# Performance work log

Measured on AMD Instinct MI355X. Metric: run time of the kernel, lower is better.

Reference implementation:

```python
import jax, jax.numpy as jnp
import numpy as np

B, L, D, H = 2, 2048, 1024, 16
Dh = D // H            # 64
DIL = 2                # dilation
WIN = 256              # window_size
HID = 4 * D            # ffn hidden (mlp_ratio=4.0)
EPS = 1e-5             # LayerNorm eps (torch default)


def _layernorm(x, w, b):
    m = jnp.mean(x, axis=-1, keepdims=True)
    v = jnp.mean(jnp.square(x - m), axis=-1, keepdims=True)
    return (x - m) * jax.lax.rsqrt(v + EPS) * w + b


def _dilated_mask(L):
    i = jnp.arange(L)[:, None]
    j = jnp.arange(L)[None, :]
    d = i - j
    return (jnp.remainder(d, DIL) == 0) & (jnp.abs(d) <= WIN) & (j <= i)  # [L,L] bool, True=allowed


def setup_inputs() -> dict:
    key = jax.random.key(0)
    ks = jax.random.split(key, 16)
    s = 0.02
    return {
        "x": jax.random.normal(ks[0], (B, L, D), jnp.float32),
        "norm1_w": jnp.ones((D,), jnp.float32),
        "norm1_b": jnp.zeros((D,), jnp.float32),
        "qkv_w": jax.random.normal(ks[1], (D, 3 * D), jnp.float32) * s,
        "qkv_b": jnp.zeros((3 * D,), jnp.float32),
        "out_w": jax.random.normal(ks[2], (D, D), jnp.float32) * s,
        "out_b": jnp.zeros((D,), jnp.float32),
        "norm2_w": jnp.ones((D,), jnp.float32),
        "norm2_b": jnp.zeros((D,), jnp.float32),
        "ffn_w1": jax.random.normal(ks[3], (D, HID), jnp.float32) * s,
        "ffn_b1": jnp.zeros((HID,), jnp.float32),
        "ffn_w2": jax.random.normal(ks[4], (HID, D), jnp.float32) * s,
        "ffn_b2": jnp.zeros((D,), jnp.float32),
    }


def reference(x, norm1_w, norm1_b, qkv_w, qkv_b, out_w, out_b,
              norm2_w, norm2_b, ffn_w1, ffn_b1, ffn_w2, ffn_b2):
    # pre-norm dilated attention block
    xn = _layernorm(x, norm1_w, norm1_b)
    qkv = xn @ qkv_w + qkv_b                         # [B,L,3D]
    q, k, v = jnp.split(qkv, 3, axis=-1)
    to_h = lambda t: t.reshape(B, L, H, Dh).transpose(0, 2, 1, 3)  # [B,H,L,Dh]
    qh, kh, vh = to_h(q), to_h(k), to_h(v)

    scale = 1.0 / jnp.sqrt(jnp.float32(Dh))
    scores = jnp.einsum('bhqd,bhkd->bhqk', qh, kh) * scale  # [B,H,L,L]
    allowed = _dilated_mask(L)                               # [L,L]
    scores = jnp.where(allowed[None, None], scores, jnp.float32(-1e30))
    p = jax.nn.softmax(scores, axis=-1)
    o = jnp.einsum('bhqk,bhkd->bhqd', p, vh)                 # [B,H,L,Dh]
    o = o.transpose(0, 2, 1, 3).reshape(B, L, D)
    attn_out = o @ out_w + out_b

    y = x + attn_out                                          # residual (dropout=0)
    h = _layernorm(y, norm2_w, norm2_b)
    h = jax.nn.gelu(h @ ffn_w1 + ffn_b1, approximate=False) @ ffn_w2 + ffn_b2
    return y + h
```

## Files before the change

kernel.cpp:

```cpp
#include <hip/hip_runtime.h>
#include <math.h>

#define BB 2
#define LL 2048
#define DD 1024
#define HH 16
#define DH 64
#define HID 4096
#define MROWS (BB*LL)

typedef __attribute__((ext_vector_type(8))) short bf16x8;
typedef __attribute__((ext_vector_type(4))) float f32x4;

__device__ __forceinline__ unsigned short f2bf(float f) {
    unsigned u = __builtin_bit_cast(unsigned, f);
    unsigned r = u + 0x7fffu + ((u >> 16) & 1u);
    return (unsigned short)(r >> 16);
}

__device__ __forceinline__ void ldsload16(const void* g, void* l) {
    __builtin_amdgcn_global_load_lds(
        (const __attribute__((address_space(1))) unsigned int*)g,
        (__attribute__((address_space(3))) unsigned int*)l,
        16, 0, 0);
}

__global__ __launch_bounds__(256) void convT_kernel(const float* __restrict__ in,
                                                    unsigned short* __restrict__ out,
                                                    int K, int N) {
    __shared__ float tile[64][65];
    int kt = blockIdx.y << 6, nt = blockIdx.x << 6;
    int t = threadIdx.x;
    int tr = t >> 4;
    int tc = (t & 15) << 2;
    #pragma unroll
    for (int i = 0; i < 4; ++i) {
        float4 v = *reinterpret_cast<const float4*>(&in[(size_t)(kt + i*16 + tr) * N + nt + tc]);
        tile[i*16 + tr][tc+0] = v.x;
        tile[i*16 + tr][tc+1] = v.y;
        tile[i*16 + tr][tc+2] = v.z;
        tile[i*16 + tr][tc+3] = v.w;
    }
    __syncthreads();
    #pragma unroll
    for (int i = 0; i < 4; ++i) {
        int n = i*16 + tr;
        ushort4 o4;
        o4.x = f2bf(tile[tc+0][n]);
        o4.y = f2bf(tile[tc+1][n]);
        o4.z = f2bf(tile[tc+2][n]);
        o4.w = f2bf(tile[tc+3][n]);
        *reinterpret_cast<ushort4*>(&out[(size_t)(nt + n) * K + kt + tc]) = o4;
    }
}

__global__ __launch_bounds__(256) void ln_kernel(const float* __restrict__ in,
                                                 const float* __restrict__ w,
                                                 const float* __restrict__ b,
                                                 unsigned short* __restrict__ out) {
    int row = blockIdx.x;
    const float* x = in + (size_t)row * DD;
    unsigned short* o = out + (size_t)row * DD;
    int t = threadIdx.x;
    float4 v = reinterpret_cast<const float4*>(x)[t];
    float s  = v.x + v.y + v.z + v.w;
    float ss = v.x*v.x + v.y*v.y + v.z*v.z + v.w*v.w;
    #pragma unroll
    for (int off = 32; off > 0; off >>= 1) {
        s  += __shfl_down(s,  off, 64);
        ss += __shfl_down(ss, off, 64);
    }
    __shared__ float red[8];
    int wid = t >> 6, lane = t & 63;
    if (lane == 0) { red[wid] = s; red[4 + wid] = ss; }
    __syncthreads();
    if (t == 0) {
        float S  = red[0] + red[1] + red[2] + red[3];
        float SS = red[4] + red[5] + red[6] + red[7];
        float mean = S / DD;
        float var  = SS / DD - mean * mean;
        red[0] = mean;
        red[1] = rsqrtf(var + 1e-5f);
    }
    __syncthreads();
    float mean = red[0], rstd = red[1];
    float4 wv = reinterpret_cast<const float4*>(w)[t];
    float4 bv = reinterpret_cast<const float4*>(b)[t];
    ushort4 ov;
    ov.x = f2bf((v.x - mean) * rstd * wv.x + bv.x);
    ov.y = f2bf((v.y - mean) * rstd * wv.y + bv.y);
    ov.z = f2bf((v.z - mean) * rstd * wv.z + bv.z);
    ov.w = f2bf((v.w - mean) * rstd * wv.w + bv.w);
    reinterpret_cast<ushort4*>(o)[t] = ov;
}

template<int EPI>
__global__ __launch_bounds__(256) void mgemm(
    const unsigned short* __restrict__ A,
    const unsigned short* __restrict__ WT,
    const float* __restrict__ bias,
    const float* res, void* Cv,
    int M, int N, int K, int nbx)
{
    __shared__ __align__(16) unsigned char smem[32768];
    int bid = blockIdx.x;
    int nwg = gridDim.x;
    int cpx = nwg >> 3;
    int swz = (bid & 7) * cpx + (bid >> 3);
    int bn = (swz % nbx) * 128;
    int bm = (swz / nbx) * 128;
    int t = threadIdx.x, lane = t & 63, w = t >> 6;
    int wr = w >> 1, wc = w & 1;
    int l15 = lane & 15, l4 = lane >> 4;

    const unsigned short* Ap = A  + (size_t)(bm + w*32 + l15) * K + 8*l4;
    const unsigned short* Bp = WT + (size_t)(bn + w*32 + l15) * K + 8*l4;
    unsigned stoff = w*2048 + lane*16;

    f32x4 acc[4][4] = {};
    int nk = K >> 5;

    {
        unsigned char* bs = smem;
        ldsload16(Ap,        bs + stoff);
        ldsload16(Ap + 16*K, bs + stoff + 1024);
        ldsload16(Bp,        bs + 8192 + stoff);
        ldsload16(Bp + 16*K, bs + 8192 + stoff + 1024);
        Ap += 32; Bp += 32;
    }
    for (int k = 0; k < nk; ++k) {
        if (k + 1 < nk) {
            unsigned char* bs = smem + (((k + 1) & 1) << 14);
            ldsload16(Ap,        bs + stoff);
            ldsload16(Ap + 16*K, bs + stoff + 1024);
            ldsload16(Bp,        bs + 8192 + stoff);
            ldsload16(Bp + 16*K, bs + 8192 + stoff + 1024);
            Ap += 32; Bp += 32;
            asm volatile("s_waitcnt vmcnt(4)\ns_barrier" ::: "memory");
        } else {
            asm volatile("s_waitcnt vmcnt(0)\ns_barrier" ::: "memory");
        }
        unsigned char* Asb = smem + ((k & 1) << 14);
        unsigned char* Bsb = Asb + 8192;
        bf16x8 af[4], bfr[4];
        #pragma unroll
        for (int mm = 0; mm < 4; ++mm)
            af[mm] = *reinterpret_cast<const bf16x8*>(Asb + (wr*4 + mm)*1024 + lane*16);
        #pragma unroll
        for (int nn = 0; nn < 4; ++nn)
            bfr[nn] = *reinterpret_cast<const bf16x8*>(Bsb + (wc*4 + nn)*1024 + lane*16);
        #pragma unroll
        for (int mm = 0; mm < 4; ++mm)
            #pragma unroll
            for (int nn = 0; nn < 4; ++nn)
                acc[mm][nn] = __builtin_amdgcn_mfma_f32_16x16x32_bf16(af[mm], bfr[nn], acc[mm][nn], 0, 0, 0);
        asm volatile("s_waitcnt lgkmcnt(0)\ns_barrier" ::: "memory");
    }

    #pragma unroll
    for (int mm = 0; mm < 4; ++mm) {
        int row0 = bm + wr*64 + mm*16 + l4*4;
        #pragma unroll
        for (int nn = 0; nn < 4; ++nn) {
            int col = bn + wc*64 + nn*16 + l15;
            float bi = bias[col];
            #pragma unroll
            for (int r = 0; r < 4; ++r) {
                float v = acc[mm][nn][r] + bi;
                size_t idx = (size_t)(row0 + r) * N + col;
                if (EPI == 0) {
                    ((float*)Cv)[idx] = v;
                } else if (EPI == 2) {
                    ((float*)Cv)[idx] = v + res[idx];
                } else {
                    v = 0.5f * v * (1.0f + erff(v * 0.70710678118654752f));
                    ((unsigned short*)Cv)[idx] = f2bf(v);
                }
            }
        }
    }
}

__global__ __launch_bounds__(128) void attn_kernel(
    const float* __restrict__ qkv,
    unsigned short* __restrict__ o)
{
    __shared__ __align__(16) float Ks[64][68];
    __shared__ __align__(16) float Vs[64][68];

    int qt = blockIdx.x;
    int p  = blockIdx.y;
    int bh = blockIdx.z;
    int b = bh >> 4, h = bh & 15;
    int t = threadIdx.x, w = t >> 6, lane = t & 63;

    const float scale = 0.125f;
    int tq = qt * 64 + lane;
    int lq = 2 * tq + p;

    const float* qrow = qkv + (size_t)(b * LL + lq) * (3 * DD) + h * DH;
    float qreg[DH];
    #pragma unroll
    for (int d = 0; d < DH; d += 4) {
        float4 t4 = *reinterpret_cast<const float4*>(qrow + d);
        qreg[d]     = t4.x * scale;
        qreg[d + 1] = t4.y * scale;
        qreg[d + 2] = t4.z * scale;
        qreg[d + 3] = t4.w * scale;
    }

    float m = 0.f, lsum = 0.f;
    float acc[DH] = {};

    int kt0 = qt - 2; if (kt0 < 0) kt0 = 0;
    for (int kt = kt0; kt <= qt; ++kt) {
        int ck = kt * 64 + lane;
        const float* src = qkv + (size_t)(b * LL + 2 * ck + p) * (3 * DD) + DD + (w ? DD : 0) + h * DH;
        float* dst = w ? &Vs[lane][0] : &Ks[lane][0];
        #pragma unroll
        for (int d = 0; d < DH; d += 4)
            *reinterpret_cast<float4*>(dst + d) = *reinterpret_cast<const float4*>(src + d);
        __syncthreads();
        for (int jj = 0; jj < 32; ++jj) {
            int j = w * 32 + jj;
            int cj = kt * 64 + j;
            const float* kr = &Ks[j][0];
            float s0 = 0.f, s1 = 0.f, s2 = 0.f, s3 = 0.f;
            #pragma unroll
            for (int d = 0; d < DH; d += 4) {
                s0 = fmaf(qreg[d],     kr[d],     s0);
                s1 = fmaf(qreg[d + 1], kr[d + 1], s1);
                s2 = fmaf(qreg[d + 2], kr[d + 2], s2);
                s3 = fmaf(qreg[d + 3], kr[d + 3], s3);
            }
            float s = (s0 + s1) + (s2 + s3);
            bool ok = (cj >= tq - 128) && (cj <= tq);
            s = ok ? s : -1e30f;
            if (s > m + 8.f) {
                float corr = __expf(m - s);
                lsum *= corr;
                #pragma unroll
                for (int d = 0; d < DH; ++d) acc[d] *= corr;
                m = s;
            }
            float pj = __expf(s - m);
            lsum += pj;
            const float* vr = &Vs[j][0];
            #pragma unroll
            for (int d = 0; d < DH; ++d) acc[d] = fmaf(pj, vr[d], acc[d]);
        }
        __syncthreads();
    }

    float* mb  = &Ks[0][0];
    float* msl = &Vs[0][0];
    if (w == 1) {
        #pragma unroll
        for (int d = 0; d < DH; d += 4) {
            float4 a4 = {acc[d], acc[d + 1], acc[d + 2], acc[d + 3]};
            *reinterpret_cast<float4*>(&mb[lane * 68 + d]) = a4;
        }
        msl[lane]      = m;
        msl[68 + lane] = lsum;
    }
    __syncthreads();
    if (w == 0) {
        float m1 = msl[lane], l1 = msl[68 + lane];
        float mx = fmaxf(m, m1);
        float c0 = __expf(m - mx), c1 = __expf(m1 - mx);
        float L  = lsum * c0 + l1 * c1;
        float inv = 1.f / L;
        unsigned short* orow = o + (size_t)(b * LL + lq) * DD + h * DH;
        #pragma unroll
        for (int d = 0; d < DH; d += 4) {
            float4 a1 = *reinterpret_cast<const float4*>(&mb[lane * 68 + d]);
            ushort4 o4;
            o4.x = f2bf((acc[d]     * c0 + a1.x * c1) * inv);
            o4.y = f2bf((acc[d + 1] * c0 + a1.y * c1) * inv);
            o4.z = f2bf((acc[d + 2] * c0 + a1.z * c1) * inv);
            o4.w = f2bf((acc[d + 3] * c0 + a1.w * c1) * inv);
            *reinterpret_cast<ushort4*>(orow + d) = o4;
        }
    }
}

extern "C" void kernel_launch(void* const* d_in, const int* in_sizes, int n_in,
                              void* d_out, int out_size, void* d_ws, size_t ws_size,
                              hipStream_t stream) {
    const float* x      = (const float*)d_in[0];
    const float* n1w    = (const float*)d_in[1];
    const float* n1b    = (const float*)d_in[2];
    const float* qkv_w  = (const float*)d_in[3];
    const float* qkv_b  = (const float*)d_in[4];
    const float* out_w  = (const float*)d_in[5];
    const float* out_b  = (const float*)d_in[6];
    const float* n2w    = (const float*)d_in[7];
    const float* n2b    = (const float*)d_in[8];
    const float* ffn_w1 = (const float*)d_in[9];
    const float* ffn_b1 = (const float*)d_in[10];
    const float* ffn_w2 = (const float*)d_in[11];
    const float* ffn_b2 = (const float*)d_in[12];

    unsigned char* wsb = (unsigned char*)d_ws;
    const size_t MB = 1024 * 1024;

    float*          qkv_buf = (float*)wsb;
    unsigned short* mid     = (unsigned short*)wsb;
    unsigned short* hbuf    = (unsigned short*)(wsb + 32*MB);
    unsigned short* xn      = (unsigned short*)(wsb + 48*MB);
    unsigned short* o_b     = xn;
    unsigned short* qkvT    = (unsigned short*)(wsb + 56*MB);
    unsigned short* outT    = qkvT + (size_t)3*1024*1024;
    unsigned short* w1T     = qkvT + (size_t)4*1024*1024;
    unsigned short* w2T     = qkvT + (size_t)8*1024*1024;
    float*          y       = (float*)d_out;

    convT_kernel<<<dim3(3*DD/64, DD/64), 256, 0, stream>>>(qkv_w,  qkvT, DD,  3*DD);
    convT_kernel<<<dim3(DD/64,   DD/64), 256, 0, stream>>>(out_w,  outT, DD,  DD);
    convT_kernel<<<dim3(HID/64,  DD/64), 256, 0, stream>>>(ffn_w1, w1T,  DD,  HID);
    convT_kernel<<<dim3(DD/64,  HID/64), 256, 0, stream>>>(ffn_w2, w2T,  HID, DD);

    ln_kernel<<<MROWS, 256, 0, stream>>>(x, n1w, n1b, xn);
    mgemm<0><<<(3*DD/128)*(MROWS/128), 256, 0, stream>>>(
        xn, qkvT, qkv_b, nullptr, qkv_buf, MROWS, 3*DD, DD, 3*DD/128);
    attn_kernel<<<dim3(16, 2, BB*HH), 128, 0, stream>>>(qkv_buf, o_b);
    mgemm<2><<<(DD/128)*(MROWS/128), 256, 0, stream>>>(
        o_b, outT, out_b, x, y, MROWS, DD, DD, DD/128);
    ln_kernel<<<MROWS, 256, 0, stream>>>(y, n2w, n2b, hbuf);
    mgemm<1><<<(HID/128)*(MROWS/128), 256, 0, stream>>>(
        hbuf, w1T, ffn_b1, nullptr, mid, MROWS, HID, DD, HID/128);
    mgemm<2><<<(DD/128)*(MROWS/128), 256, 0, stream>>>(
        mid, w2T, ffn_b2, y, y, MROWS, DD, HID, DD/128);
}
```

Measured before the change: 454.1 us.

## Use MFMA attention with bf16 QKV, transposed V, and triple-buffered GEMM

The attention kernel is rewritten to compute QK^T and PV with bf16 MFMA instructions, using a swizzled LDS tile for P, in place of scalar fp32 FMA loops. The QKV GEMM epilogue now writes bf16 Q/K and scatters V into a per-head, parity-split transposed layout, which halves QKV traffic and feeds MFMA operands directly. All GEMMs move from double to triple buffering of LDS tiles so global loads are prefetched two steps ahead. The costs are more shared memory per GEMM block, which may lower occupancy, bf16 rounding of Q/K/V and P, and a scattered V store.

```diff
diff --git a/kernel.cpp b/kernel.cpp
--- a/kernel.cpp
+++ b/kernel.cpp
@@ -100,9 +100,10 @@
     const unsigned short* __restrict__ WT,
     const float* __restrict__ bias,
     const float* res, void* Cv,
+    unsigned short* __restrict__ vt,
     int M, int N, int K, int nbx)
 {
-    __shared__ __align__(16) unsigned char smem[32768];
+    __shared__ __align__(16) unsigned char smem[49152];
     int bid = blockIdx.x;
     int nwg = gridDim.x;
     int cpx = nwg >> 3;
@@ -120,28 +121,32 @@
     f32x4 acc[4][4] = {};
     int nk = K >> 5;
 
-    {
-        unsigned char* bs = smem;
+    unsigned char* pb0 = smem;
+    unsigned char* pb1 = smem + 16384;
+    unsigned char* pb2 = smem + 32768;
+
+    auto stage = [&](unsigned char* bs) {
         ldsload16(Ap,        bs + stoff);
         ldsload16(Ap + 16*K, bs + stoff + 1024);
         ldsload16(Bp,        bs + 8192 + stoff);
         ldsload16(Bp + 16*K, bs + 8192 + stoff + 1024);
         Ap += 32; Bp += 32;
-    }
+    };
+
+    stage(pb0);
+    stage(pb1);
+
     for (int k = 0; k < nk; ++k) {
-        if (k + 1 < nk) {
-            unsigned char* bs = smem + (((k + 1) & 1) << 14);
-            ldsload16(Ap,        bs + stoff);
-            ldsload16(Ap + 16*K, bs + stoff + 1024);
-            ldsload16(Bp,        bs + 8192 + stoff);
-            ldsload16(Bp + 16*K, bs + 8192 + stoff + 1024);
-            Ap += 32; Bp += 32;
+        if (k + 2 < nk) {
+            stage(pb2);
+            asm volatile("s_waitcnt vmcnt(8)\ns_barrier" ::: "memory");
+        } else if (k + 2 == nk) {
             asm volatile("s_waitcnt vmcnt(4)\ns_barrier" ::: "memory");
         } else {
             asm volatile("s_waitcnt vmcnt(0)\ns_barrier" ::: "memory");
         }
-        unsigned char* Asb = smem + ((k & 1) << 14);
-        unsigned char* Bsb = Asb + 8192;
+        unsigned char* Asb = pb0;
+        unsigned char* Bsb = pb0 + 8192;
         bf16x8 af[4], bfr[4];
         #pragma unroll
         for (int mm = 0; mm < 4; ++mm)
@@ -155,8 +160,10 @@
             for (int nn = 0; nn < 4; ++nn)
                 acc[mm][nn] = __builtin_amdgcn_mfma_f32_16x16x32_bf16(af[mm], bfr[nn], acc[mm][nn], 0, 0, 0);
         asm volatile("s_waitcnt lgkmcnt(0)\ns_barrier" ::: "memory");
-    }
-
+        unsigned char* tp = pb0; pb0 = pb1; pb1 = pb2; pb2 = tp;
+    }
+
+    bool isv = (EPI == 3) && (bn >= 2048);
     #pragma unroll
     for (int mm = 0; mm < 4; ++mm) {
         int row0 = bm + wr*64 + mm*16 + l4*4;
@@ -167,119 +174,147 @@
             #pragma unroll
             for (int r = 0; r < 4; ++r) {
                 float v = acc[mm][nn][r] + bi;
-                size_t idx = (size_t)(row0 + r) * N + col;
-                if (EPI == 0) {
-                    ((float*)Cv)[idx] = v;
-                } else if (EPI == 2) {
+                int row = row0 + r;
+                size_t idx = (size_t)row * N + col;
+                if (EPI == 2) {
                     ((float*)Cv)[idx] = v + res[idx];
-                } else {
+                } else if (EPI == 1) {
                     v = 0.5f * v * (1.0f + erff(v * 0.70710678118654752f));
                     ((unsigned short*)Cv)[idx] = f2bf(v);
+                } else {
+                    if (!isv) {
+                        ((unsigned short*)Cv)[idx] = f2bf(v);
+                    } else {
+                        int bb = row >> 11, l = row & 2047;
+                        int c2 = col - 2048, hh = c2 >> 6, dd = c2 & 63;
+                        vt[((((size_t)(bb*HH + hh)*2 + (l & 1))*64 + dd) << 10) + (l >> 1)] = f2bf(v);
+                    }
                 }
             }
         }
     }
 }
 
-__global__ __launch_bounds__(128) void attn_kernel(
-    const float* __restrict__ qkv,
+__global__ __launch_bounds__(64, 1) void mattn(
+    const unsigned short* __restrict__ qkvb,
+    const unsigned short* __restrict__ vt,
     unsigned short* __restrict__ o)
 {
-    __shared__ __align__(16) float Ks[64][68];
-    __shared__ __align__(16) float Vs[64][68];
-
-    int qt = blockIdx.x;
-    int p  = blockIdx.y;
-    int bh = blockIdx.z;
+    __shared__ __align__(16) unsigned char PlB[8192];
+    int qt = blockIdx.x, p = blockIdx.y, bh = blockIdx.z;
     int b = bh >> 4, h = bh & 15;
-    int t = threadIdx.x, w = t >> 6, lane = t & 63;
-
-    const float scale = 0.125f;
-    int tq = qt * 64 + lane;
-    int lq = 2 * tq + p;
-
-    const float* qrow = qkv + (size_t)(b * LL + lq) * (3 * DD) + h * DH;
-    float qreg[DH];
-    #pragma unroll
-    for (int d = 0; d < DH; d += 4) {
-        float4 t4 = *reinterpret_cast<const float4*>(qrow + d);
-        qreg[d]     = t4.x * scale;
-        qreg[d + 1] = t4.y * scale;
-        qreg[d + 2] = t4.z * scale;
-        qreg[d + 3] = t4.w * scale;
-    }
-
-    float m = 0.f, lsum = 0.f;
-    float acc[DH] = {};
+    int lane = threadIdx.x;
+    int l15 = lane & 15, l4 = lane >> 4;
+
+    bf16x8 qf[4][2];
+    #pragma unroll
+    for (int qb = 0; qb < 4; ++qb) {
+        int tq = qt*64 + qb*16 + l15;
+        const unsigned short* qr = qkvb + (size_t)(b*LL + 2*tq + p)*3072 + h*64 + 8*l4;
+        qf[qb][0] = *reinterpret_cast<const bf16x8*>(qr);
+        qf[qb][1] = *reinterpret_cast<const bf16x8*>(qr + 32);
+    }
+
+    float mreg[4], lreg[4];
+    #pragma unroll
+    for (int qb = 0; qb < 4; ++qb) { mreg[qb] = -1e30f; lreg[qb] = 0.f; }
+    f32x4 oac[4][4] = {};
+
+    const unsigned short* vbase = vt + ((size_t)((b*HH + h)*2 + p) << 16);
 
     int kt0 = qt - 2; if (kt0 < 0) kt0 = 0;
     for (int kt = kt0; kt <= qt; ++kt) {
-        int ck = kt * 64 + lane;
-        const float* src = qkv + (size_t)(b * LL + 2 * ck + p) * (3 * DD) + DD + (w ? DD : 0) + h * DH;
-        float* dst = w ? &Vs[lane][0] : &Ks[lane][0];
-        #pragma unroll
-        for (int d = 0; d < DH; d += 4)
-            *reinterpret_cast<float4*>(dst + d) = *reinterpret_cast<const float4*>(src + d);
-        __syncthreads();
-        for (int jj = 0; jj < 32; ++jj) {
-            int j = w * 32 + jj;
-            int cj = kt * 64 + j;
-            const float* kr = &Ks[j][0];
-            float s0 = 0.f, s1 = 0.f, s2 = 0.f, s3 = 0.f;
-            #pragma unroll
-            for (int d = 0; d < DH; d += 4) {
-                s0 = fmaf(qreg[d],     kr[d],     s0);
-                s1 = fmaf(qreg[d + 1], kr[d + 1], s1);
-                s2 = fmaf(qreg[d + 2], kr[d + 2], s2);
-                s3 = fmaf(qreg[d + 3], kr[d + 3], s3);
-            }
-            float s = (s0 + s1) + (s2 + s3);
-            bool ok = (cj >= tq - 128) && (cj <= tq);
-            s = ok ? s : -1e30f;
-            if (s > m + 8.f) {
-                float corr = __expf(m - s);
-                lsum *= corr;
+        bf16x8 kf[4][2], vf[4][2];
+        #pragma unroll
+        for (int kb = 0; kb < 4; ++kb) {
+            const unsigned short* kr = qkvb + (size_t)(b*LL + 2*(kt*64 + kb*16 + l15) + p)*3072 + 1024 + h*64 + 8*l4;
+            kf[kb][0] = *reinterpret_cast<const bf16x8*>(kr);
+            kf[kb][1] = *reinterpret_cast<const bf16x8*>(kr + 32);
+        }
+        #pragma unroll
+        for (int mt = 0; mt < 4; ++mt) {
+            const unsigned short* vr = vbase + (mt*16 + l15)*1024 + kt*64 + 8*l4;
+            vf[mt][0] = *reinterpret_cast<const bf16x8*>(vr);
+            vf[mt][1] = *reinterpret_cast<const bf16x8*>(vr + 32);
+        }
+        f32x4 st[4][4];
+        #pragma unroll
+        for (int kb = 0; kb < 4; ++kb)
+            #pragma unroll
+            for (int qb = 0; qb < 4; ++qb) {
+                f32x4 z = {0.f, 0.f, 0.f, 0.f};
+                z = __builtin_amdgcn_mfma_f32_16x16x32_bf16(kf[kb][0], qf[qb][0], z, 0, 0, 0);
+                st[kb][qb] = __builtin_amdgcn_mfma_f32_16x16x32_bf16(kf[kb][1], qf[qb][1], z, 0, 0, 0);
+            }
+        #pragma unroll
+        for (int qb = 0; qb < 4; ++qb) {
+            int tq = qt*64 + qb*16 + l15;
+            int q = qb*16 + l15;
+            float tmax = -1e30f;
+            #pragma unroll
+            for (int kb = 0; kb < 4; ++kb)
                 #pragma unroll
-                for (int d = 0; d < DH; ++d) acc[d] *= corr;
-                m = s;
-            }
-            float pj = __expf(s - m);
-            lsum += pj;
-            const float* vr = &Vs[j][0];
-            #pragma unroll
-            for (int d = 0; d < DH; ++d) acc[d] = fmaf(pj, vr[d], acc[d]);
-        }
-        __syncthreads();
-    }
-
-    float* mb  = &Ks[0][0];
-    float* msl = &Vs[0][0];
-    if (w == 1) {
-        #pragma unroll
-        for (int d = 0; d < DH; d += 4) {
-            float4 a4 = {acc[d], acc[d + 1], acc[d + 2], acc[d + 3]};
-            *reinterpret_cast<float4*>(&mb[lane * 68 + d]) = a4;
-        }
-        msl[lane]      = m;
-        msl[68 + lane] = lsum;
-    }
-    __syncthreads();
-    if (w == 0) {
-        float m1 = msl[lane], l1 = msl[68 + lane];
-        float mx = fmaxf(m, m1);
-        float c0 = __expf(m - mx), c1 = __expf(m1 - mx);
-        float L  = lsum * c0 + l1 * c1;
-        float inv = 1.f / L;
-        unsigned short* orow = o + (size_t)(b * LL + lq) * DD + h * DH;
-        #pragma unroll
-        for (int d = 0; d < DH; d += 4) {
-            float4 a1 = *reinterpret_cast<const float4*>(&mb[lane * 68 + d]);
+                for (int r = 0; r < 4; ++r) {
+                    int kc = kt*64 + kb*16 + 4*l4 + r;
+                    float sv = st[kb][qb][r] * 0.125f;
+                    sv = (kc + 128 >= tq && kc <= tq) ? sv : -1e30f;
+                    st[kb][qb][r] = sv;
+                    tmax = fmaxf(tmax, sv);
+                }
+            tmax = fmaxf(tmax, __shfl_xor(tmax, 16, 64));
+            tmax = fmaxf(tmax, __shfl_xor(tmax, 32, 64));
+            float newm = fmaxf(mreg[qb], tmax);
+            float corr = __expf(mreg[qb] - newm);
+            mreg[qb] = newm;
+            float ps = 0.f;
+            #pragma unroll
+            for (int kb = 0; kb < 4; ++kb) {
+                float p0 = __expf(st[kb][qb][0] - newm);
+                float p1 = __expf(st[kb][qb][1] - newm);
+                float p2 = __expf(st[kb][qb][2] - newm);
+                float p3 = __expf(st[kb][qb][3] - newm);
+                ps += (p0 + p1) + (p2 + p3);
+                unsigned lo = (unsigned)f2bf(p0) | ((unsigned)f2bf(p1) << 16);
+                unsigned hi = (unsigned)f2bf(p2) | ((unsigned)f2bf(p3) << 16);
+                unsigned byteoff = ((unsigned)(q << 7) + (unsigned)(kb*32 + 8*l4)) ^ ((unsigned)(q & 7) << 4);
+                *reinterpret_cast<uint2*>(PlB + byteoff) = make_uint2(lo, hi);
+            }
+            ps += __shfl_xor(ps, 16, 64);
+            ps += __shfl_xor(ps, 32, 64);
+            lreg[qb] = lreg[qb] * corr + ps;
+            #pragma unroll
+            for (int mt = 0; mt < 4; ++mt) {
+                oac[mt][qb][0] *= corr; oac[mt][qb][1] *= corr;
+                oac[mt][qb][2] *= corr; oac[mt][qb][3] *= corr;
+            }
+        }
+        #pragma unroll
+        for (int c = 0; c < 2; ++c)
+            #pragma unroll
+            for (int qb = 0; qb < 4; ++qb) {
+                int q = qb*16 + l15;
+                unsigned rb = ((unsigned)(q << 7) + (unsigned)(c*64 + 16*l4)) ^ ((unsigned)(q & 7) << 4);
+                bf16x8 pf = *reinterpret_cast<const bf16x8*>(PlB + rb);
+                #pragma unroll
+                for (int mt = 0; mt < 4; ++mt)
+                    oac[mt][qb] = __builtin_amdgcn_mfma_f32_16x16x32_bf16(vf[mt][c], pf, oac[mt][qb], 0, 0, 0);
+            }
+    }
+
+    #pragma unroll
+    for (int qb = 0; qb < 4; ++qb) {
+        float inv = 1.f / lreg[qb];
+        int tq = qt*64 + qb*16 + l15;
+        unsigned short* orow = o + (size_t)(b*LL + 2*tq + p)*DD + h*64;
+        #pragma unroll
+        for (int mt = 0; mt < 4; ++mt) {
+            int d0 = mt*16 + 4*l4;
             ushort4 o4;
-            o4.x = f2bf((acc[d]     * c0 + a1.x * c1) * inv);
-            o4.y = f2bf((acc[d + 1] * c0 + a1.y * c1) * inv);
-            o4.z = f2bf((acc[d + 2] * c0 + a1.z * c1) * inv);
-            o4.w = f2bf((acc[d + 3] * c0 + a1.w * c1) * inv);
-            *reinterpret_cast<ushort4*>(orow + d) = o4;
+            o4.x = f2bf(oac[mt][qb][0] * inv);
+            o4.y = f2bf(oac[mt][qb][1] * inv);
+            o4.z = f2bf(oac[mt][qb][2] * inv);
+            o4.w = f2bf(oac[mt][qb][3] * inv);
+            *reinterpret_cast<ushort4*>(orow + d0) = o4;
         }
     }
 }
@@ -304,16 +339,17 @@
     unsigned char* wsb = (unsigned char*)d_ws;
     const size_t MB = 1024 * 1024;
 
-    float*          qkv_buf = (float*)wsb;
-    unsigned short* mid     = (unsigned short*)wsb;
-    unsigned short* hbuf    = (unsigned short*)(wsb + 32*MB);
-    unsigned short* xn      = (unsigned short*)(wsb + 48*MB);
-    unsigned short* o_b     = xn;
-    unsigned short* qkvT    = (unsigned short*)(wsb + 56*MB);
-    unsigned short* outT    = qkvT + (size_t)3*1024*1024;
-    unsigned short* w1T     = qkvT + (size_t)4*1024*1024;
-    unsigned short* w2T     = qkvT + (size_t)8*1024*1024;
-    float*          y       = (float*)d_out;
+    unsigned short* qkvb = (unsigned short*)wsb;
+    unsigned short* vt   = (unsigned short*)(wsb + 24*MB);
+    unsigned short* mid  = (unsigned short*)wsb;
+    unsigned short* o_b  = (unsigned short*)(wsb + 32*MB);
+    unsigned short* xn   = (unsigned short*)(wsb + 40*MB);
+    unsigned short* hbuf = (unsigned short*)(wsb + 48*MB);
+    unsigned short* qkvT = (unsigned short*)(wsb + 56*MB);
+    unsigned short* outT = (unsigned short*)(wsb + 62*MB);
+    unsigned short* w1T  = (unsigned short*)(wsb + 64*MB);
+    unsigned short* w2T  = (unsigned short*)(wsb + 72*MB);
+    float*          y    = (float*)d_out;
 
     convT_kernel<<<dim3(3*DD/64, DD/64), 256, 0, stream>>>(qkv_w,  qkvT, DD,  3*DD);
     convT_kernel<<<dim3(DD/64,   DD/64), 256, 0, stream>>>(out_w,  outT, DD,  DD);
@@ -321,14 +357,14 @@
     convT_kernel<<<dim3(DD/64,  HID/64), 256, 0, stream>>>(ffn_w2, w2T,  HID, DD);
 
     ln_kernel<<<MROWS, 256, 0, stream>>>(x, n1w, n1b, xn);
-    mgemm<0><<<(3*DD/128)*(MROWS/128), 256, 0, stream>>>(
-        xn, qkvT, qkv_b, nullptr, qkv_buf, MROWS, 3*DD, DD, 3*DD/128);
-    attn_kernel<<<dim3(16, 2, BB*HH), 128, 0, stream>>>(qkv_buf, o_b);
+    mgemm<3><<<(3*DD/128)*(MROWS/128), 256, 0, stream>>>(
+        xn, qkvT, qkv_b, nullptr, qkvb, vt, MROWS, 3*DD, DD, 3*DD/128);
+    mattn<<<dim3(16, 2, BB*HH), 64, 0, stream>>>(qkvb, vt, o_b);
     mgemm<2><<<(DD/128)*(MROWS/128), 256, 0, stream>>>(
-        o_b, outT, out_b, x, y, MROWS, DD, DD, DD/128);
+        o_b, outT, out_b, x, y, nullptr, MROWS, DD, DD, DD/128);
     ln_kernel<<<MROWS, 256, 0, stream>>>(y, n2w, n2b, hbuf);
     mgemm<1><<<(HID/128)*(MROWS/128), 256, 0, stream>>>(
-        hbuf, w1T, ffn_b1, nullptr, mid, MROWS, HID, DD, HID/128);
+        hbuf, w1T, ffn_b1, nullptr, mid, nullptr, MROWS, HID, DD, HID/128);
     mgemm<2><<<(DD/128)*(MROWS/128), 256, 0, stream>>>(
-        mid, w2T, ffn_b2, y, y, MROWS, DD, HID, DD/128);
-}
+        mid, w2T, ffn_b2, y, y, nullptr, MROWS, DD, HID, DD/128);
+}
```

Result: faster. 388.0 us (-14.6%).
